# Kernel optimization log

Hardware: AMD Instinct MI355X
Metric: run time of the kernel (lower is better)

## Reference

```python
import jax, jax.numpy as jnp
import numpy as np

B, P, E = 256, 196, 2048           # batch, num_pixels, encoder_size
H, A, EMB = 2048, 512, 300         # hidden, attention, embedding dims
V_IN, V_OUT = 262, 261             # input vocab (classes+2), output (classes+1)
T = 7                              # max_seq_len + 2


def setup_inputs() -> dict:
    key = jax.random.key(0)
    ks = jax.random.split(key, 20)
    s = 0.02
    return {
        "encoder_feature_out": jax.random.normal(ks[0], (B, P, E), jnp.float32),
        "encoder_out": jax.random.normal(ks[1], (B, E), jnp.float32),
        "annotations_X": jax.random.randint(ks[2], (B, T), 0, V_IN),
        "is_train": 1,
        "emb_W": jax.random.normal(ks[3], (V_IN, EMB), jnp.float32) * s,
        "feat_W": jax.random.normal(ks[4], (H, E), jnp.float32) * s,
        "feat_b": jnp.zeros((H,), jnp.float32),
        "W_ih": jax.random.normal(ks[5], (4 * H, EMB + E), jnp.float32) * s,
        "W_hh": jax.random.normal(ks[6], (4 * H, H), jnp.float32) * s,
        "b_ih": jnp.zeros((4 * H,), jnp.float32),
        "b_hh": jnp.zeros((4 * H,), jnp.float32),
        "enc_att_W": jax.random.normal(ks[7], (A, E), jnp.float32) * s,
        "enc_att_b": jnp.zeros((A,), jnp.float32),
        "dec_att_W": jax.random.normal(ks[8], (A, H), jnp.float32) * s,
        "dec_att_b": jnp.zeros((A,), jnp.float32),
        "full_att_W": jax.random.normal(ks[9], (1, A), jnp.float32) * s,
        "full_att_b": jnp.zeros((1,), jnp.float32),
        "fbeta_W": jax.random.normal(ks[10], (E, H), jnp.float32) * s,
        "fbeta_b": jnp.zeros((E,), jnp.float32),
        "fc_W": jax.random.normal(ks[11], (V_OUT, H), jnp.float32) * s,
        "fc_b": jnp.zeros((V_OUT,), jnp.float32),
    }


def _forward(encoder_feature_out, encoder_out, annotations_X,
             emb_W, feat_W, feat_b, W_ih, W_hh, b_ih, b_hh,
             enc_att_W, enc_att_b, dec_att_W, dec_att_b,
             full_att_W, full_att_b, fbeta_W, fbeta_b, fc_W, fc_b):
    enc = encoder_feature_out                                  # (B,P,E)
    # encoder side of additive attention is constant across steps
    att1 = jnp.einsum('bpe,ae->bpa', enc, enc_att_W) + enc_att_b  # (B,P,A)
    h0 = encoder_out @ feat_W.T + feat_b                       # (B,H)
    c0 = jnp.zeros_like(h0)

    def step(carry, ann_t):
        h, c = carry
        # additive attention
        att2 = h @ dec_att_W.T + dec_att_b                     # (B,A)
        e = jax.nn.relu(att1 + att2[:, None, :]) @ full_att_W[0] + full_att_b[0]  # (B,P)
        alpha = jax.nn.softmax(e, axis=1)                      # (B,P)
        awe = jnp.einsum('bp,bpe->be', alpha, enc)             # (B,E)
        gate = jax.nn.sigmoid(h @ fbeta_W.T + fbeta_b)         # (B,E)
        awe = gate * awe
        # LSTMCell (dropout layers in eval mode -> identity)
        x = jnp.concatenate([emb_W[ann_t], awe], axis=1)       # (B,EMB+E)
        gates = x @ W_ih.T + b_ih + h @ W_hh.T + b_hh          # (B,4H)
        i, f, g, o = jnp.split(gates, 4, axis=1)
        c = jax.nn.sigmoid(f) * c + jax.nn.sigmoid(i) * jnp.tanh(g)
        h = jax.nn.sigmoid(o) * jnp.tanh(c)
        yhat = h @ fc_W.T + fc_b                               # (B,V_OUT)
        return (h, c), (yhat, alpha)

    _, (yhats, alphas) = jax.lax.scan(step, (h0, c0), annotations_X.T)  # (T,B,...)
    return jnp.transpose(yhats, (1, 0, 2)), jnp.transpose(alphas, (1, 0, 2))


def reference(encoder_feature_out, encoder_out, annotations_X, is_train,
              emb_W, feat_W, feat_b, W_ih, W_hh, b_ih, b_hh,
              enc_att_W, enc_att_b, dec_att_W, dec_att_b,
              full_att_W, full_att_b, fbeta_W, fbeta_b, fc_W, fc_b):
    # is_train=True (teacher forcing) path
    return _forward(encoder_feature_out, encoder_out, annotations_X,
                    emb_W, feat_W, feat_b, W_ih, W_hh, b_ih, b_hh,
                    enc_att_W, enc_att_b, dec_att_W, dec_att_b,
                    full_att_W, full_att_b, fbeta_W, fbeta_b, fc_W, fc_b)
```

## Files before the change

kernel.cpp:

```cpp
#include <hip/hip_runtime.h>
#include <math.h>

#define B_    256
#define P_    196
#define E_    2048
#define H_    2048
#define A_    512
#define EMB_  300
#define VOUT_ 261
#define T_    7

#define KPAD_   4608
#define EMBOFF_ 2048
#define AWEOFF_ 2352

#define NSTEP_  2880
#define FCOFF_  2560
#define GSPLIT_ 4

typedef __attribute__((ext_vector_type(8))) short          short8_t;
typedef __attribute__((ext_vector_type(8))) unsigned short ushort8_t;
typedef __attribute__((ext_vector_type(4))) float          f32x4;

__device__ __forceinline__ unsigned short f2b(float f) {
    union { float f; unsigned int u; } v; v.f = f;
    unsigned int x = v.u;
    unsigned int r = (x + 0x7fffu + ((x >> 16) & 1u)) >> 16;
    return (unsigned short)r;
}
__device__ __forceinline__ float b2f(unsigned short u) {
    union { unsigned int u; float f; } v; v.u = ((unsigned int)u) << 16;
    return v.f;
}
__device__ __forceinline__ ushort8_t pack8(float4 u0, float4 u1) {
    ushort8_t u;
    u[0]=f2b(u0.x); u[1]=f2b(u0.y); u[2]=f2b(u0.z); u[3]=f2b(u0.w);
    u[4]=f2b(u1.x); u[5]=f2b(u1.y); u[6]=f2b(u1.z); u[7]=f2b(u1.w);
    return u;
}

template<bool SPLITK, bool OUT16, bool XCDSWZ>
__global__ __launch_bounds__(256)
void gemm_sk(const unsigned short* __restrict__ Ab, int lda,
             const unsigned short* __restrict__ Bw, int ldb,
             void* __restrict__ Cout, int ldc,
             int Kper, int colbase, const float* __restrict__ bias, int nbx)
{
    __shared__ ushort8_t As8[256 * 8];
    __shared__ ushort8_t Bs8[64 * 8];

    const int tid  = threadIdx.x;
    const int lane = tid & 63;
    const int w    = tid >> 6;

    int nblk, mblk;
    if (XCDSWZ) {
        const int bid  = blockIdx.x;
        const int pair = (bid & 7) * (gridDim.x >> 3) + (bid >> 3);
        nblk = pair % nbx;
        mblk = pair / nbx;
    } else {
        nblk = blockIdx.x;
        mblk = 0;
    }
    const int col0  = colbase + nblk * 64;
    const int kbase = SPLITK ? blockIdx.y * Kper : 0;
    const int mrow0 = XCDSWZ ? mblk * 256 : 0;

    const int rb  = tid >> 3;
    const int seg = tid & 7;
    const int swz = seg ^ (rb & 7);

    const unsigned short* Ap = Ab + (size_t)(mrow0 + rb) * lda + kbase + seg * 8;
    const unsigned short* Bp = Bw + (size_t)(col0 + rb) * ldb + kbase + seg * 8;

    const int lr = lane & 15;
    const int hi = lane >> 4;

    f32x4 acc[4][4];
    #pragma unroll
    for (int m = 0; m < 4; ++m)
        #pragma unroll
        for (int n = 0; n < 4; ++n)
            acc[m][n] = (f32x4){0.f, 0.f, 0.f, 0.f};

    ushort8_t aR[8], bR[2];
    #pragma unroll
    for (int i = 0; i < 8; ++i)
        aR[i] = *(const ushort8_t*)(Ap + (size_t)i * 32 * lda);
    bR[0] = *(const ushort8_t*)(Bp);
    bR[1] = *(const ushort8_t*)(Bp + (size_t)32 * ldb);

    for (int k0 = 0; k0 < Kper; k0 += 64) {
        __syncthreads();
        #pragma unroll
        for (int i = 0; i < 8; ++i)
            As8[(rb + i * 32) * 8 + swz] = aR[i];
        Bs8[rb * 8 + swz]        = bR[0];
        Bs8[(rb + 32) * 8 + swz] = bR[1];
        __syncthreads();
        if (k0 + 64 < Kper) {
            #pragma unroll
            for (int i = 0; i < 8; ++i)
                aR[i] = *(const ushort8_t*)(Ap + (size_t)i * 32 * lda + k0 + 64);
            bR[0] = *(const ushort8_t*)(Bp + k0 + 64);
            bR[1] = *(const ushort8_t*)(Bp + (size_t)32 * ldb + k0 + 64);
        }
        #pragma unroll
        for (int kc = 0; kc < 2; ++kc) {
            short8_t af[4], bf[4];
            #pragma unroll
            for (int m = 0; m < 4; ++m) {
                const int row = w * 64 + m * 16 + lr;
                af[m] = *(const short8_t*)&As8[row * 8 + ((kc * 4 + hi) ^ (row & 7))];
            }
            #pragma unroll
            for (int n = 0; n < 4; ++n) {
                const int row = n * 16 + lr;
                bf[n] = *(const short8_t*)&Bs8[row * 8 + ((kc * 4 + hi) ^ (row & 7))];
            }
            #pragma unroll
            for (int m = 0; m < 4; ++m)
                #pragma unroll
                for (int n = 0; n < 4; ++n)
                    acc[m][n] = __builtin_amdgcn_mfma_f32_16x16x32_bf16(
                        af[m], bf[n], acc[m][n], 0, 0, 0);
        }
    }

    if (OUT16) {
        unsigned short* C16 = (unsigned short*)Cout;
        #pragma unroll
        for (int m = 0; m < 4; ++m) {
            const int grow0 = mrow0 + w * 64 + m * 16 + hi * 4;
            #pragma unroll
            for (int n = 0; n < 4; ++n) {
                const int gcol = col0 + n * 16 + lr;
                const float bv = bias[gcol];
                #pragma unroll
                for (int r = 0; r < 4; ++r)
                    C16[(size_t)(grow0 + r) * ldc + gcol] = f2b(acc[m][n][r] + bv);
            }
        }
    } else {
        float* Cs = (float*)Cout + (SPLITK ? (size_t)blockIdx.y * 256 * ldc : 0);
        #pragma unroll
        for (int m = 0; m < 4; ++m) {
            const int grow0 = w * 64 + m * 16 + hi * 4;
            #pragma unroll
            for (int n = 0; n < 4; ++n) {
                const int gcol = col0 + n * 16 + lr;
                #pragma unroll
                for (int r = 0; r < 4; ++r)
                    Cs[(size_t)(grow0 + r) * ldc + gcol] = acc[m][n][r];
            }
        }
    }
}

__global__ __launch_bounds__(256)
void gemm_mfma_f32(const float* __restrict__ Af, int lda,
                   const unsigned short* __restrict__ Bw, int ldb,
                   unsigned short* __restrict__ Cp, int ldc,
                   const float* __restrict__ bias,
                   int M, int N, int K)
{
    __shared__ __align__(16) unsigned short As[64][40];
    __shared__ __align__(16) unsigned short Bs[128][40];

    const int tid  = threadIdx.x;
    const int lane = tid & 63;
    const int wid  = tid >> 6;
    const int wr   = wid >> 1;
    const int wc   = wid & 1;
    const int row0 = blockIdx.y * 64;
    const int col0 = blockIdx.x * 128;

    const int ar = tid >> 2;
    const int as = (tid & 3) * 8;
    const int br = tid >> 1;
    const int bs = (tid & 1) * 16;

    const int lr = lane & 15;
    const int lk = (lane >> 4) * 8;

    f32x4 acc[2][4];
    #pragma unroll
    for (int m = 0; m < 2; ++m)
        #pragma unroll
        for (int n = 0; n < 4; ++n)
            acc[m][n] = (f32x4){0.f, 0.f, 0.f, 0.f};

    for (int k0 = 0; k0 < K; k0 += 32) {
        ushort8_t aval = {0,0,0,0,0,0,0,0};
        if (row0 + ar < M) {
            const float* p = Af + (size_t)(row0 + ar) * lda + k0 + as;
            aval = pack8(*(const float4*)(p), *(const float4*)(p + 4));
        }
        ushort8_t bv0 = {0,0,0,0,0,0,0,0}, bv1 = {0,0,0,0,0,0,0,0};
        if (col0 + br < N) {
            const unsigned short* p = Bw + (size_t)(col0 + br) * ldb + k0 + bs;
            bv0 = *(const ushort8_t*)(p);
            bv1 = *(const ushort8_t*)(p + 8);
        }
        __syncthreads();
        *(ushort8_t*)&As[ar][as]     = aval;
        *(ushort8_t*)&Bs[br][bs]     = bv0;
        *(ushort8_t*)&Bs[br][bs + 8] = bv1;
        __syncthreads();

        short8_t af[2], bf[4];
        #pragma unroll
        for (int m = 0; m < 2; ++m)
            af[m] = *(const short8_t*)&As[wr * 32 + m * 16 + lr][lk];
        #pragma unroll
        for (int n = 0; n < 4; ++n)
            bf[n] = *(const short8_t*)&Bs[wc * 64 + n * 16 + lr][lk];
        #pragma unroll
        for (int m = 0; m < 2; ++m)
            #pragma unroll
            for (int n = 0; n < 4; ++n)
                acc[m][n] = __builtin_amdgcn_mfma_f32_16x16x32_bf16(
                    af[m], bf[n], acc[m][n], 0, 0, 0);
    }

    #pragma unroll
    for (int m = 0; m < 2; ++m) {
        const int grow0 = row0 + wr * 32 + m * 16 + (lane >> 4) * 4;
        #pragma unroll
        for (int n = 0; n < 4; ++n) {
            const int gcol = col0 + wc * 64 + n * 16 + lr;
            if (gcol >= N) continue;
            const float bv = bias[gcol];
            #pragma unroll
            for (int r = 0; r < 4; ++r) {
                const int grow = grow0 + r;
                if (grow >= M) continue;
                Cp[(size_t)grow * ldc + gcol] = f2b(acc[m][n][r] + bv);
            }
        }
    }
}

__global__ __launch_bounds__(256)
void cvt_bf16_kernel(const float* __restrict__ in, unsigned short* __restrict__ out,
                     int n8)
{
    const int idx = blockIdx.x * 256 + threadIdx.x;
    if (idx >= n8) return;
    const size_t base = (size_t)idx * 8;
    *(ushort8_t*)(out + base) =
        pack8(*(const float4*)(in + base), *(const float4*)(in + base + 4));
}

__global__ __launch_bounds__(256)
void build_wcat_kernel(const float* __restrict__ W_ih, const float* __restrict__ W_hh,
                       unsigned short* __restrict__ wcat)
{
    const int row = blockIdx.x;
    const int LIH = EMB_ + E_;
    for (int s = threadIdx.x; s < KPAD_ / 8; s += 256) {
        const int k0 = s * 8;
        ushort8_t u;
        const float* src = nullptr;
        if (k0 + 8 <= H_)                         src = W_hh + (size_t)row * H_ + k0;
        else if (k0 >= H_ && k0 + 8 <= 2344)      src = W_ih + (size_t)row * LIH + (k0 - H_);
        else if (k0 >= AWEOFF_ && k0 + 8 <= 4400) src = W_ih + (size_t)row * LIH + (k0 - 2052);
        if (src) {
            u = pack8(*(const float4*)(src), *(const float4*)(src + 4));
        } else {
            #pragma unroll
            for (int i = 0; i < 8; ++i) {
                const int k = k0 + i;
                float v = 0.f;
                if (k >= H_ && k < 2348)           v = W_ih[(size_t)row * LIH + (k - H_)];
                else if (k >= AWEOFF_ && k < 4400) v = W_ih[(size_t)row * LIH + (k - 2052)];
                u[i] = f2b(v);
            }
        }
        *(ushort8_t*)(wcat + (size_t)row * KPAD_ + k0) = u;
    }
}

__global__ __launch_bounds__(256)
void build_wstep_kernel(const float* __restrict__ dec_attW,
                        const float* __restrict__ fbeta_W,
                        const float* __restrict__ fc_W,
                        unsigned short* __restrict__ wstep)
{
    const int row = blockIdx.x;
    const int c0  = threadIdx.x * 8;
    const float* src;
    if (row < A_)                   src = dec_attW + (size_t)row * H_ + c0;
    else if (row < A_ + E_)         src = fbeta_W + (size_t)(row - A_) * H_ + c0;
    else if (row < A_ + E_ + VOUT_) src = fc_W + (size_t)(row - A_ - E_) * H_ + c0;
    else                            src = nullptr;
    ushort8_t u = {0,0,0,0,0,0,0,0};
    if (src) u = pack8(*(const float4*)(src), *(const float4*)(src + 4));
    *(ushort8_t*)(wstep + (size_t)row * H_ + c0) = u;
}

__global__ __launch_bounds__(256)
void reduce_h0(const float* __restrict__ parts, const float* __restrict__ bias,
               unsigned short* __restrict__ xcat)
{
    const int i = blockIdx.x * 256 + threadIdx.x;
    const int row = i >> 11, col = i & (H_ - 1);
    float acc = bias[col];
    #pragma unroll
    for (int s = 0; s < 8; ++s)
        acc += parts[(size_t)s * 256 * H_ + i];
    xcat[(size_t)row * KPAD_ + col] = f2b(acc);
}

__global__ __launch_bounds__(256)
void fused_att(const float* __restrict__ parts, const float* __restrict__ dec_attb,
               const unsigned short* __restrict__ att1,
               const float* __restrict__ fw_g, const float* __restrict__ fb,
               float* __restrict__ alpha, float* __restrict__ out_a, int t)
{
    const int b = blockIdx.x;
    const int tid = threadIdx.x;
    const int lane = tid & 63;
    const int wid  = tid >> 6;
    __shared__ float att2s[A_];
    __shared__ float es[P_];
    __shared__ float red[4];

    #pragma unroll
    for (int it = 0; it < A_ / 256; ++it) {
        const int c = tid + it * 256;
        float acc = dec_attb[c];
        #pragma unroll
        for (int s = 0; s < 8; ++s)
            acc += parts[((size_t)s * B_ + b) * NSTEP_ + c];
        att2s[c] = acc;
    }
    __syncthreads();

    const int l32  = lane & 31;
    const int slot = wid * 2 + (lane >> 5);
    float a2r[16], fwr[16];
    #pragma unroll
    for (int k = 0; k < 16; ++k) {
        a2r[k] = att2s[l32 * 16 + k];
        fwr[k] = fw_g[l32 * 16 + k];
    }
    const float fbv = fb[0];

    for (int p = slot; p < P_; p += 8) {
        const unsigned short* row = att1 + ((size_t)b * P_ + p) * A_ + l32 * 16;
        ushort8_t v0 = *(const ushort8_t*)(row);
        ushort8_t v1 = *(const ushort8_t*)(row + 8);
        float acc = 0.f;
        #pragma unroll
        for (int k = 0; k < 8; ++k) {
            float x = b2f(v0[k]) + a2r[k];
            x = x > 0.f ? x : 0.f;
            acc = fmaf(x, fwr[k], acc);
        }
        #pragma unroll
        for (int k = 0; k < 8; ++k) {
            float x = b2f(v1[k]) + a2r[k + 8];
            x = x > 0.f ? x : 0.f;
            acc = fmaf(x, fwr[k + 8], acc);
        }
        #pragma unroll
        for (int off = 16; off > 0; off >>= 1)
            acc += __shfl_xor(acc, off);
        if (l32 == 0) es[p] = acc + fbv;
    }
    __syncthreads();

    float v = (tid < P_) ? es[tid] : -1e30f;
    float m = v;
    #pragma unroll
    for (int off = 32; off > 0; off >>= 1)
        m = fmaxf(m, __shfl_xor(m, off));
    if (lane == 0) red[wid] = m;
    __syncthreads();
    m = fmaxf(fmaxf(red[0], red[1]), fmaxf(red[2], red[3]));
    __syncthreads();
    float p = (tid < P_) ? expf(v - m) : 0.f;
    float s = p;
    #pragma unroll
    for (int off = 32; off > 0; off >>= 1)
        s += __shfl_xor(s, off);
    if (lane == 0) red[wid] = s;
    __syncthreads();
    s = red[0] + red[1] + red[2] + red[3];
    if (tid < P_) {
        const float a = p / s;
        alpha[b * P_ + tid] = a;
        out_a[((size_t)b * T_ + t) * P_ + tid] = a;
    }
}

__global__ __launch_bounds__(256)
void fused_awe(const float* __restrict__ parts, const float* __restrict__ fbeta_b,
               const float* __restrict__ alpha,
               const float* __restrict__ encf, const unsigned short* __restrict__ enc16,
               int use16,
               const int* __restrict__ ann, const float* __restrict__ embW,
               unsigned short* __restrict__ xcat,
               const float* __restrict__ fc_b, float* __restrict__ out_y, int t)
{
    const int b = blockIdx.x;
    const int tid = threadIdx.x;
    __shared__ float al[P_];
    if (tid < P_) al[tid] = alpha[b * P_ + tid];
    __syncthreads();

    const int e0 = tid * 8;
    float g[8];
    #pragma unroll
    for (int k = 0; k < 8; ++k) {
        float acc = fbeta_b[e0 + k];
        #pragma unroll
        for (int s = 0; s < 8; ++s)
            acc += parts[((size_t)s * B_ + b) * NSTEP_ + A_ + e0 + k];
        g[k] = 1.f / (1.f + expf(-acc));
    }

    float acc[8] = {0.f,0.f,0.f,0.f,0.f,0.f,0.f,0.f};
    if (use16) {
        const unsigned short* ep = enc16 + (size_t)b * P_ * E_ + e0;
        for (int p = 0; p < P_; p += 4) {
            ushort8_t v0 = *(const ushort8_t*)(ep + (size_t)(p + 0) * E_);
            ushort8_t v1 = *(const ushort8_t*)(ep + (size_t)(p + 1) * E_);
            ushort8_t v2 = *(const ushort8_t*)(ep + (size_t)(p + 2) * E_);
            ushort8_t v3 = *(const ushort8_t*)(ep + (size_t)(p + 3) * E_);
            const float a0 = al[p], a1 = al[p + 1], a2 = al[p + 2], a3 = al[p + 3];
            #pragma unroll
            for (int k = 0; k < 8; ++k) {
                float t0 = fmaf(a0, b2f(v0[k]), acc[k]);
                float t1 = fmaf(a1, b2f(v1[k]), t0);
                float t2 = fmaf(a2, b2f(v2[k]), t1);
                acc[k]   = fmaf(a3, b2f(v3[k]), t2);
            }
        }
    } else {
        const float* ep = encf + (size_t)b * P_ * E_ + e0;
        for (int p = 0; p < P_; ++p) {
            float4 v0 = *(const float4*)(ep + (size_t)p * E_);
            float4 v1 = *(const float4*)(ep + (size_t)p * E_ + 4);
            const float a0 = al[p];
            acc[0] = fmaf(a0, v0.x, acc[0]); acc[1] = fmaf(a0, v0.y, acc[1]);
            acc[2] = fmaf(a0, v0.z, acc[2]); acc[3] = fmaf(a0, v0.w, acc[3]);
            acc[4] = fmaf(a0, v1.x, acc[4]); acc[5] = fmaf(a0, v1.y, acc[5]);
            acc[6] = fmaf(a0, v1.z, acc[6]); acc[7] = fmaf(a0, v1.w, acc[7]);
        }
    }
    ushort8_t o;
    #pragma unroll
    for (int k = 0; k < 8; ++k) o[k] = f2b(g[k] * acc[k]);
    *(ushort8_t*)(xcat + (size_t)b * KPAD_ + AWEOFF_ + e0) = o;

    const int r = ann[b * T_ + t];
    for (int j = tid; j < EMB_; j += 256)
        xcat[(size_t)b * KPAD_ + EMBOFF_ + j] = f2b(embW[(size_t)r * EMB_ + j]);

    if (t > 0) {
        for (int c = tid; c < VOUT_; c += 256) {
            float a = fc_b[c];
            #pragma unroll
            for (int s = 0; s < 8; ++s)
                a += parts[((size_t)s * B_ + b) * NSTEP_ + FCOFF_ + c];
            out_y[((size_t)b * T_ + (t - 1)) * VOUT_ + c] = a;
        }
    }
}

__global__ __launch_bounds__(256)
void fc_reduce(const float* __restrict__ parts, const float* __restrict__ fc_b,
               float* __restrict__ out_y, int tm1)
{
    const int i = blockIdx.x * 256 + threadIdx.x;
    if (i >= B_ * VOUT_) return;
    const int b = i / VOUT_;
    const int c = i - b * VOUT_;
    float acc = fc_b[c];
    #pragma unroll
    for (int s = 0; s < 8; ++s)
        acc += parts[((size_t)s * B_ + b) * NSTEP_ + FCOFF_ + c];
    out_y[((size_t)b * T_ + tm1) * VOUT_ + c] = acc;
}

__global__ __launch_bounds__(256)
void lstm_kernel(const float* __restrict__ parts, const float* __restrict__ bias4h,
                 float* __restrict__ c, unsigned short* __restrict__ xcat)
{
    const int idx = blockIdx.x * 256 + threadIdx.x;
    const int b = idx >> 11;
    const int j = idx & (H_ - 1);
    const float* p0 = parts + (size_t)b * 4 * H_;
    const size_t S = (size_t)256 * 4 * H_;
    float gi = bias4h[j],          gf = bias4h[H_ + j];
    float gg = bias4h[2 * H_ + j], go = bias4h[3 * H_ + j];
    #pragma unroll
    for (int s = 0; s < GSPLIT_; ++s) {
        const float* p = p0 + s * S;
        gi += p[j]; gf += p[H_ + j]; gg += p[2 * H_ + j]; go += p[3 * H_ + j];
    }
    const float si = 1.f / (1.f + expf(-gi));
    const float sf = 1.f / (1.f + expf(-gf));
    const float so = 1.f / (1.f + expf(-go));
    const float cn = sf * c[idx] + si * tanhf(gg);
    c[idx] = cn;
    xcat[(size_t)b * KPAD_ + j] = f2b(so * tanhf(cn));
}

__global__ __launch_bounds__(256)
void addvec_kernel(const float* __restrict__ a, const float* __restrict__ b,
                   float* __restrict__ o, int n)
{
    const int i = blockIdx.x * 256 + threadIdx.x;
    if (i < n) o[i] = a[i] + b[i];
}

extern "C" void kernel_launch(void* const* d_in, const int* in_sizes, int n_in,
                              void* d_out, int out_size, void* d_ws, size_t ws_size,
                              hipStream_t stream)
{
    const float* enc      = (const float*)d_in[0];
    const float* enc_out  = (const float*)d_in[1];
    const int*   ann      = (const int*)  d_in[2];
    const float* emb_W    = (const float*)d_in[4];
    const float* feat_W   = (const float*)d_in[5];
    const float* feat_b   = (const float*)d_in[6];
    const float* W_ih     = (const float*)d_in[7];
    const float* W_hh     = (const float*)d_in[8];
    const float* b_ih     = (const float*)d_in[9];
    const float* b_hh     = (const float*)d_in[10];
    const float* enc_attW = (const float*)d_in[11];
    const float* enc_attb = (const float*)d_in[12];
    const float* dec_attW = (const float*)d_in[13];
    const float* dec_attb = (const float*)d_in[14];
    const float* full_attW= (const float*)d_in[15];
    const float* full_attb= (const float*)d_in[16];
    const float* fbeta_W  = (const float*)d_in[17];
    const float* fbeta_b  = (const float*)d_in[18];
    const float* fc_W     = (const float*)d_in[19];
    const float* fc_b     = (const float*)d_in[20];
    (void)in_sizes; (void)n_in; (void)out_size;

    float* out   = (float*)d_out;
    float* out_y = out;
    float* out_a = out + (size_t)B_ * T_ * VOUT_;

    char* base = (char*)d_ws;
    size_t off = 0;
    auto alloc = [&](size_t bytes) -> char* {
        char* p = base + off;
        off += (bytes + 255) & ~(size_t)255;
        return p;
    };
    unsigned short* att1_16   = (unsigned short*)alloc((size_t)B_ * P_ * A_ * 2);
    unsigned short* wcat16    = (unsigned short*)alloc((size_t)4 * H_ * KPAD_ * 2);
    unsigned short* wstep16   = (unsigned short*)alloc((size_t)NSTEP_ * H_ * 2);
    unsigned short* encattW16 = (unsigned short*)alloc((size_t)A_ * E_ * 2);
    unsigned short* featW16   = (unsigned short*)alloc((size_t)H_ * E_ * 2);
    unsigned short* encout16  = (unsigned short*)alloc((size_t)B_ * E_ * 2);
    unsigned short* xcat16    = (unsigned short*)alloc((size_t)B_ * KPAD_ * 2);
    float* cbuf    = (float*)alloc((size_t)B_ * H_ * 4);
    float* alpha   = (float*)alloc((size_t)B_ * P_ * 4);
    float* bias4h  = (float*)alloc((size_t)4 * H_ * 4);
    const size_t parts_elems = (size_t)GSPLIT_ * B_ * 4 * H_;
    float* parts   = (float*)alloc(parts_elems * 4);
    const size_t enc_elems = (size_t)B_ * P_ * E_;
    const int use16 = (off + enc_elems * 2 <= ws_size) ? 1 : 0;
    unsigned short* enc16 = use16 ? (unsigned short*)alloc(enc_elems * 2) : nullptr;

    const dim3 blk(256);

    addvec_kernel<<<dim3((4 * H_ + 255) / 256), blk, 0, stream>>>(b_ih, b_hh, bias4h, 4 * H_);
    cvt_bf16_kernel<<<dim3((A_ * E_ / 8 + 255) / 256), blk, 0, stream>>>(enc_attW, encattW16, A_ * E_ / 8);
    cvt_bf16_kernel<<<dim3((H_ * E_ / 8 + 255) / 256), blk, 0, stream>>>(feat_W, featW16, H_ * E_ / 8);
    cvt_bf16_kernel<<<dim3((B_ * E_ / 8 + 255) / 256), blk, 0, stream>>>(enc_out, encout16, B_ * E_ / 8);
    build_wcat_kernel<<<dim3(4 * H_), blk, 0, stream>>>(W_ih, W_hh, wcat16);
    build_wstep_kernel<<<dim3(NSTEP_), blk, 0, stream>>>(dec_attW, fbeta_W, fc_W, wstep16);
    hipMemsetAsync(xcat16, 0, (size_t)B_ * KPAD_ * 2, stream);
    hipMemsetAsync(cbuf, 0, (size_t)B_ * H_ * 4, stream);
    if (use16)
        cvt_bf16_kernel<<<dim3((int)(enc_elems / 8 + 255) / 256), blk, 0, stream>>>(
            enc, enc16, (int)(enc_elems / 8));

    if (use16) {
        gemm_sk<false, true, true><<<dim3(196 * 8), blk, 0, stream>>>(
            enc16, E_, encattW16, E_, att1_16, A_, E_, 0, enc_attb, 8);
    } else {
        dim3 g((A_ + 127) / 128, (B_ * P_) / 64);
        gemm_mfma_f32<<<g, blk, 0, stream>>>(enc, E_, encattW16, E_,
            att1_16, A_, enc_attb, B_ * P_, A_, E_);
    }
    gemm_sk<true, false, false><<<dim3(H_ / 64, 8), blk, 0, stream>>>(
        encout16, E_, featW16, E_, parts, H_, E_ / 8, 0, nullptr, 0);
    reduce_h0<<<dim3(B_ * H_ / 256), blk, 0, stream>>>(parts, feat_b, xcat16);

    for (int t = 0; t <= T_; ++t) {
        if (t < T_)
            gemm_sk<true, false, false><<<dim3(NSTEP_ / 64, 8), blk, 0, stream>>>(
                xcat16, KPAD_, wstep16, H_, parts, NSTEP_, H_ / 8, 0, nullptr, 0);
        else
            gemm_sk<true, false, false><<<dim3((NSTEP_ - FCOFF_) / 64, 8), blk, 0, stream>>>(
                xcat16, KPAD_, wstep16, H_, parts, NSTEP_, H_ / 8, FCOFF_, nullptr, 0);
        if (t == T_) {
            fc_reduce<<<dim3((B_ * VOUT_ + 255) / 256), blk, 0, stream>>>(parts, fc_b, out_y, t - 1);
            break;
        }

        fused_att<<<dim3(B_), blk, 0, stream>>>(parts, dec_attb, att1_16,
                                                full_attW, full_attb, alpha, out_a, t);
        fused_awe<<<dim3(B_), blk, 0, stream>>>(parts, fbeta_b, alpha, enc, enc16,
                                                use16, ann, emb_W, xcat16,
                                                fc_b, out_y, t);

        gemm_sk<true, false, false><<<dim3(4 * H_ / 64, GSPLIT_), blk, 0, stream>>>(
            xcat16, KPAD_, wcat16, KPAD_, parts, 4 * H_, KPAD_ / GSPLIT_, 0, nullptr, 0);
        lstm_kernel<<<dim3(B_ * H_ / 256), blk, 0, stream>>>(parts, bias4h, cbuf, xcat16);
    }
}
```

Baseline: 1.226 ms.

## Split attention-weighted encoding across pixel halves and widen att1 GEMM tile

The fused attention-weighted-encoding kernel is split in two. One kernel computes partial sums over two halves of the pixel range, using 2×B blocks instead of B, and a second kernel reduces the halves and applies the sigmoid gate. This is meant to give more parallelism to the bandwidth-bound encoder read in each step. Separately, the gemm kernel gains a template parameter for N tile width, and the one-time encoder attention projection now uses 128-wide tiles to improve A-tile reuse. Costs are an extra launch per step, an extra buffer round-trip, and more registers in the wider GEMM.

```diff
diff --git a/kernel.cpp b/kernel.cpp
--- a/kernel.cpp
+++ b/kernel.cpp
@@ -39,15 +39,17 @@
     return u;
 }
 
-template<bool SPLITK, bool OUT16, bool XCDSWZ>
+template<bool SPLITK, bool OUT16, bool XCDSWZ, int BN>
 __global__ __launch_bounds__(256)
 void gemm_sk(const unsigned short* __restrict__ Ab, int lda,
              const unsigned short* __restrict__ Bw, int ldb,
              void* __restrict__ Cout, int ldc,
              int Kper, int colbase, const float* __restrict__ bias, int nbx)
 {
+    constexpr int NB32 = BN / 32;
+    constexpr int NF   = BN / 16;
     __shared__ ushort8_t As8[256 * 8];
-    __shared__ ushort8_t Bs8[64 * 8];
+    __shared__ ushort8_t Bs8[BN * 8];
 
     const int tid  = threadIdx.x;
     const int lane = tid & 63;
@@ -63,7 +65,7 @@
         nblk = blockIdx.x;
         mblk = 0;
     }
-    const int col0  = colbase + nblk * 64;
+    const int col0  = colbase + nblk * BN;
     const int kbase = SPLITK ? blockIdx.y * Kper : 0;
     const int mrow0 = XCDSWZ ? mblk * 256 : 0;
 
@@ -77,52 +79,55 @@
     const int lr = lane & 15;
     const int hi = lane >> 4;
 
-    f32x4 acc[4][4];
+    f32x4 acc[4][NF];
     #pragma unroll
     for (int m = 0; m < 4; ++m)
         #pragma unroll
-        for (int n = 0; n < 4; ++n)
+        for (int n = 0; n < NF; ++n)
             acc[m][n] = (f32x4){0.f, 0.f, 0.f, 0.f};
 
-    ushort8_t aR[8], bR[2];
+    ushort8_t aR[8], bR[NB32];
     #pragma unroll
     for (int i = 0; i < 8; ++i)
         aR[i] = *(const ushort8_t*)(Ap + (size_t)i * 32 * lda);
-    bR[0] = *(const ushort8_t*)(Bp);
-    bR[1] = *(const ushort8_t*)(Bp + (size_t)32 * ldb);
+    #pragma unroll
+    for (int j = 0; j < NB32; ++j)
+        bR[j] = *(const ushort8_t*)(Bp + (size_t)j * 32 * ldb);
 
     for (int k0 = 0; k0 < Kper; k0 += 64) {
         __syncthreads();
         #pragma unroll
         for (int i = 0; i < 8; ++i)
             As8[(rb + i * 32) * 8 + swz] = aR[i];
-        Bs8[rb * 8 + swz]        = bR[0];
-        Bs8[(rb + 32) * 8 + swz] = bR[1];
+        #pragma unroll
+        for (int j = 0; j < NB32; ++j)
+            Bs8[(rb + j * 32) * 8 + swz] = bR[j];
         __syncthreads();
         if (k0 + 64 < Kper) {
             #pragma unroll
             for (int i = 0; i < 8; ++i)
                 aR[i] = *(const ushort8_t*)(Ap + (size_t)i * 32 * lda + k0 + 64);
-            bR[0] = *(const ushort8_t*)(Bp + k0 + 64);
-            bR[1] = *(const ushort8_t*)(Bp + (size_t)32 * ldb + k0 + 64);
+            #pragma unroll
+            for (int j = 0; j < NB32; ++j)
+                bR[j] = *(const ushort8_t*)(Bp + (size_t)j * 32 * ldb + k0 + 64);
         }
         #pragma unroll
         for (int kc = 0; kc < 2; ++kc) {
-            short8_t af[4], bf[4];
+            short8_t af[4], bf[NF];
             #pragma unroll
             for (int m = 0; m < 4; ++m) {
                 const int row = w * 64 + m * 16 + lr;
                 af[m] = *(const short8_t*)&As8[row * 8 + ((kc * 4 + hi) ^ (row & 7))];
             }
             #pragma unroll
-            for (int n = 0; n < 4; ++n) {
+            for (int n = 0; n < NF; ++n) {
                 const int row = n * 16 + lr;
                 bf[n] = *(const short8_t*)&Bs8[row * 8 + ((kc * 4 + hi) ^ (row & 7))];
             }
             #pragma unroll
             for (int m = 0; m < 4; ++m)
                 #pragma unroll
-                for (int n = 0; n < 4; ++n)
+                for (int n = 0; n < NF; ++n)
                     acc[m][n] = __builtin_amdgcn_mfma_f32_16x16x32_bf16(
                         af[m], bf[n], acc[m][n], 0, 0, 0);
         }
@@ -134,7 +139,7 @@
         for (int m = 0; m < 4; ++m) {
             const int grow0 = mrow0 + w * 64 + m * 16 + hi * 4;
             #pragma unroll
-            for (int n = 0; n < 4; ++n) {
+            for (int n = 0; n < NF; ++n) {
                 const int gcol = col0 + n * 16 + lr;
                 const float bv = bias[gcol];
                 #pragma unroll
@@ -148,7 +153,7 @@
         for (int m = 0; m < 4; ++m) {
             const int grow0 = w * 64 + m * 16 + hi * 4;
             #pragma unroll
-            for (int n = 0; n < 4; ++n) {
+            for (int n = 0; n < NF; ++n) {
                 const int gcol = col0 + n * 16 + lr;
                 #pragma unroll
                 for (int r = 0; r < 4; ++r)
@@ -397,35 +402,24 @@
 }
 
 __global__ __launch_bounds__(256)
-void fused_awe(const float* __restrict__ parts, const float* __restrict__ fbeta_b,
-               const float* __restrict__ alpha,
-               const float* __restrict__ encf, const unsigned short* __restrict__ enc16,
-               int use16,
-               const int* __restrict__ ann, const float* __restrict__ embW,
-               unsigned short* __restrict__ xcat,
-               const float* __restrict__ fc_b, float* __restrict__ out_y, int t)
-{
-    const int b = blockIdx.x;
+void awe_part_kernel(const float* __restrict__ alpha,
+                     const float* __restrict__ encf,
+                     const unsigned short* __restrict__ enc16, int use16,
+                     float* __restrict__ awe_part)
+{
+    const int ph = blockIdx.x;
+    const int b  = blockIdx.y;
     const int tid = threadIdx.x;
-    __shared__ float al[P_];
-    if (tid < P_) al[tid] = alpha[b * P_ + tid];
+    __shared__ float al[98];
+    if (tid < 98) al[tid] = alpha[b * P_ + ph * 98 + tid];
     __syncthreads();
 
     const int e0 = tid * 8;
-    float g[8];
-    #pragma unroll
-    for (int k = 0; k < 8; ++k) {
-        float acc = fbeta_b[e0 + k];
-        #pragma unroll
-        for (int s = 0; s < 8; ++s)
-            acc += parts[((size_t)s * B_ + b) * NSTEP_ + A_ + e0 + k];
-        g[k] = 1.f / (1.f + expf(-acc));
-    }
-
     float acc[8] = {0.f,0.f,0.f,0.f,0.f,0.f,0.f,0.f};
     if (use16) {
-        const unsigned short* ep = enc16 + (size_t)b * P_ * E_ + e0;
-        for (int p = 0; p < P_; p += 4) {
+        const unsigned short* ep = enc16 + ((size_t)b * P_ + ph * 98) * E_ + e0;
+        int p = 0;
+        for (; p + 4 <= 98; p += 4) {
             ushort8_t v0 = *(const ushort8_t*)(ep + (size_t)(p + 0) * E_);
             ushort8_t v1 = *(const ushort8_t*)(ep + (size_t)(p + 1) * E_);
             ushort8_t v2 = *(const ushort8_t*)(ep + (size_t)(p + 2) * E_);
@@ -439,9 +433,16 @@
                 acc[k]   = fmaf(a3, b2f(v3[k]), t2);
             }
         }
+        for (; p < 98; ++p) {
+            ushort8_t v0 = *(const ushort8_t*)(ep + (size_t)p * E_);
+            const float a0 = al[p];
+            #pragma unroll
+            for (int k = 0; k < 8; ++k)
+                acc[k] = fmaf(a0, b2f(v0[k]), acc[k]);
+        }
     } else {
-        const float* ep = encf + (size_t)b * P_ * E_ + e0;
-        for (int p = 0; p < P_; ++p) {
+        const float* ep = encf + ((size_t)b * P_ + ph * 98) * E_ + e0;
+        for (int p = 0; p < 98; ++p) {
             float4 v0 = *(const float4*)(ep + (size_t)p * E_);
             float4 v1 = *(const float4*)(ep + (size_t)p * E_ + 4);
             const float a0 = al[p];
@@ -451,9 +452,39 @@
             acc[6] = fmaf(a0, v1.z, acc[6]); acc[7] = fmaf(a0, v1.w, acc[7]);
         }
     }
+    float* dst = awe_part + ((size_t)ph * B_ + b) * E_ + e0;
+    *(float4*)(dst)     = make_float4(acc[0], acc[1], acc[2], acc[3]);
+    *(float4*)(dst + 4) = make_float4(acc[4], acc[5], acc[6], acc[7]);
+}
+
+__global__ __launch_bounds__(256)
+void awe_fin_kernel(const float* __restrict__ parts, const float* __restrict__ fbeta_b,
+                    const float* __restrict__ awe_part,
+                    const int* __restrict__ ann, const float* __restrict__ embW,
+                    unsigned short* __restrict__ xcat,
+                    const float* __restrict__ fc_b, float* __restrict__ out_y, int t)
+{
+    const int b = blockIdx.x;
+    const int tid = threadIdx.x;
+    const int e0 = tid * 8;
+
+    float4 p0a = *(const float4*)(awe_part + (size_t)b * E_ + e0);
+    float4 p0b = *(const float4*)(awe_part + (size_t)b * E_ + e0 + 4);
+    float4 p1a = *(const float4*)(awe_part + ((size_t)B_ + b) * E_ + e0);
+    float4 p1b = *(const float4*)(awe_part + ((size_t)B_ + b) * E_ + e0 + 4);
+    float aw[8] = {p0a.x + p1a.x, p0a.y + p1a.y, p0a.z + p1a.z, p0a.w + p1a.w,
+                   p0b.x + p1b.x, p0b.y + p1b.y, p0b.z + p1b.z, p0b.w + p1b.w};
+
     ushort8_t o;
     #pragma unroll
-    for (int k = 0; k < 8; ++k) o[k] = f2b(g[k] * acc[k]);
+    for (int k = 0; k < 8; ++k) {
+        float g = fbeta_b[e0 + k];
+        #pragma unroll
+        for (int s = 0; s < 8; ++s)
+            g += parts[((size_t)s * B_ + b) * NSTEP_ + A_ + e0 + k];
+        const float sg = 1.f / (1.f + expf(-g));
+        o[k] = f2b(sg * aw[k]);
+    }
     *(ushort8_t*)(xcat + (size_t)b * KPAD_ + AWEOFF_ + e0) = o;
 
     const int r = ann[b * T_ + t];
@@ -562,9 +593,10 @@
     unsigned short* featW16   = (unsigned short*)alloc((size_t)H_ * E_ * 2);
     unsigned short* encout16  = (unsigned short*)alloc((size_t)B_ * E_ * 2);
     unsigned short* xcat16    = (unsigned short*)alloc((size_t)B_ * KPAD_ * 2);
-    float* cbuf    = (float*)alloc((size_t)B_ * H_ * 4);
-    float* alpha   = (float*)alloc((size_t)B_ * P_ * 4);
-    float* bias4h  = (float*)alloc((size_t)4 * H_ * 4);
+    float* cbuf     = (float*)alloc((size_t)B_ * H_ * 4);
+    float* alpha    = (float*)alloc((size_t)B_ * P_ * 4);
+    float* bias4h   = (float*)alloc((size_t)4 * H_ * 4);
+    float* awe_part = (float*)alloc((size_t)2 * B_ * E_ * 4);
     const size_t parts_elems = (size_t)GSPLIT_ * B_ * 4 * H_;
     float* parts   = (float*)alloc(parts_elems * 4);
     const size_t enc_elems = (size_t)B_ * P_ * E_;
@@ -586,23 +618,23 @@
             enc, enc16, (int)(enc_elems / 8));
 
     if (use16) {
-        gemm_sk<false, true, true><<<dim3(196 * 8), blk, 0, stream>>>(
-            enc16, E_, encattW16, E_, att1_16, A_, E_, 0, enc_attb, 8);
+        gemm_sk<false, true, true, 128><<<dim3(196 * 4), blk, 0, stream>>>(
+            enc16, E_, encattW16, E_, att1_16, A_, E_, 0, enc_attb, 4);
     } else {
         dim3 g((A_ + 127) / 128, (B_ * P_) / 64);
         gemm_mfma_f32<<<g, blk, 0, stream>>>(enc, E_, encattW16, E_,
             att1_16, A_, enc_attb, B_ * P_, A_, E_);
     }
-    gemm_sk<true, false, false><<<dim3(H_ / 64, 8), blk, 0, stream>>>(
+    gemm_sk<true, false, false, 64><<<dim3(H_ / 64, 8), blk, 0, stream>>>(
         encout16, E_, featW16, E_, parts, H_, E_ / 8, 0, nullptr, 0);
     reduce_h0<<<dim3(B_ * H_ / 256), blk, 0, stream>>>(parts, feat_b, xcat16);
 
     for (int t = 0; t <= T_; ++t) {
         if (t < T_)
-            gemm_sk<true, false, false><<<dim3(NSTEP_ / 64, 8), blk, 0, stream>>>(
+            gemm_sk<true, false, false, 64><<<dim3(NSTEP_ / 64, 8), blk, 0, stream>>>(
                 xcat16, KPAD_, wstep16, H_, parts, NSTEP_, H_ / 8, 0, nullptr, 0);
         else
-            gemm_sk<true, false, false><<<dim3((NSTEP_ - FCOFF_) / 64, 8), blk, 0, stream>>>(
+            gemm_sk<true, false, false, 64><<<dim3((NSTEP_ - FCOFF_) / 64, 8), blk, 0, stream>>>(
                 xcat16, KPAD_, wstep16, H_, parts, NSTEP_, H_ / 8, FCOFF_, nullptr, 0);
         if (t == T_) {
             fc_reduce<<<dim3((B_ * VOUT_ + 255) / 256), blk, 0, stream>>>(parts, fc_b, out_y, t - 1);
@@ -611,11 +643,11 @@
 
         fused_att<<<dim3(B_), blk, 0, stream>>>(parts, dec_attb, att1_16,
                                                 full_attW, full_attb, alpha, out_a, t);
-        fused_awe<<<dim3(B_), blk, 0, stream>>>(parts, fbeta_b, alpha, enc, enc16,
-                                                use16, ann, emb_W, xcat16,
-                                                fc_b, out_y, t);
-
-        gemm_sk<true, false, false><<<dim3(4 * H_ / 64, GSPLIT_), blk, 0, stream>>>(
+        awe_part_kernel<<<dim3(2, B_), blk, 0, stream>>>(alpha, enc, enc16, use16, awe_part);
+        awe_fin_kernel<<<dim3(B_), blk, 0, stream>>>(parts, fbeta_b, awe_part,
+                                                     ann, emb_W, xcat16, fc_b, out_y, t);
+
+        gemm_sk<true, false, false, 64><<<dim3(4 * H_ / 64, GSPLIT_), blk, 0, stream>>>(
             xcat16, KPAD_, wcat16, KPAD_, parts, 4 * H_, KPAD_ / GSPLIT_, 0, nullptr, 0);
         lstm_kernel<<<dim3(B_ * H_ / 256), blk, 0, stream>>>(parts, bias4h, cbuf, xcat16);
     }
```

Measured after the change: 1.254 ms. 2.3% more time.

## Fuse attention softmax with weighted-sum over split pixel halves; merge setup kernels

Applied to the files above, without the earlier changes.

The attention-score/softmax kernel now also computes the attention-weighted encoder sum, with the grid split into two pixel halves per batch row so 512 blocks run instead of 256. A small finishing kernel adds the two partial sums, applies the sigmoid gate and writes the LSTM input, which removes the alpha round trip through global memory. Each half-block recomputes the full softmax, so that work is duplicated. Separately, the bias add, weight conversions and buffer memsets are merged into one setup kernel to cut launch count.

```diff
diff --git a/kernel.cpp b/kernel.cpp
--- a/kernel.cpp
+++ b/kernel.cpp
@@ -17,6 +17,7 @@
 #define NSTEP_  2880
 #define FCOFF_  2560
 #define GSPLIT_ 4
+#define PSPLIT_ 2
 
 typedef __attribute__((ext_vector_type(8))) short          short8_t;
 typedef __attribute__((ext_vector_type(8))) unsigned short ushort8_t;
@@ -251,6 +252,72 @@
     const size_t base = (size_t)idx * 8;
     *(ushort8_t*)(out + base) =
         pack8(*(const float4*)(in + base), *(const float4*)(in + base + 4));
+}
+
+__global__ __launch_bounds__(256)
+void setup_kernel(const float* __restrict__ b_ih, const float* __restrict__ b_hh,
+                  float* __restrict__ bias4h,
+                  const float* __restrict__ enc_attW, unsigned short* __restrict__ encattW16,
+                  const float* __restrict__ feat_W, unsigned short* __restrict__ featW16,
+                  const float* __restrict__ enc_out, unsigned short* __restrict__ encout16,
+                  const float* __restrict__ dec_attW, const float* __restrict__ fbeta_W,
+                  const float* __restrict__ fc_W, unsigned short* __restrict__ wstep,
+                  unsigned short* __restrict__ xcat, float* __restrict__ cbuf)
+{
+    int bid = blockIdx.x;
+    const int tid = threadIdx.x;
+    if (bid < 32) {
+        const int i = bid * 256 + tid;
+        bias4h[i] = b_ih[i] + b_hh[i];
+        return;
+    }
+    bid -= 32;
+    if (bid < 512) {
+        const size_t base = ((size_t)bid * 256 + tid) * 8;
+        *(ushort8_t*)(encattW16 + base) =
+            pack8(*(const float4*)(enc_attW + base), *(const float4*)(enc_attW + base + 4));
+        return;
+    }
+    bid -= 512;
+    if (bid < 2048) {
+        const size_t base = ((size_t)bid * 256 + tid) * 8;
+        *(ushort8_t*)(featW16 + base) =
+            pack8(*(const float4*)(feat_W + base), *(const float4*)(feat_W + base + 4));
+        return;
+    }
+    bid -= 2048;
+    if (bid < 256) {
+        const size_t base = ((size_t)bid * 256 + tid) * 8;
+        *(ushort8_t*)(encout16 + base) =
+            pack8(*(const float4*)(enc_out + base), *(const float4*)(enc_out + base + 4));
+        return;
+    }
+    bid -= 256;
+    if (bid < NSTEP_) {
+        const int row = bid;
+        const int c0  = tid * 8;
+        const float* src;
+        if (row < A_)                   src = dec_attW + (size_t)row * H_ + c0;
+        else if (row < A_ + E_)         src = fbeta_W + (size_t)(row - A_) * H_ + c0;
+        else if (row < A_ + E_ + VOUT_) src = fc_W + (size_t)(row - A_ - E_) * H_ + c0;
+        else                            src = nullptr;
+        ushort8_t u = {0,0,0,0,0,0,0,0};
+        if (src) u = pack8(*(const float4*)(src), *(const float4*)(src + 4));
+        *(ushort8_t*)(wstep + (size_t)row * H_ + c0) = u;
+        return;
+    }
+    bid -= NSTEP_;
+    if (bid < 576) {
+        const size_t base = ((size_t)bid * 256 + tid) * 8;
+        ushort8_t z = {0,0,0,0,0,0,0,0};
+        *(ushort8_t*)(xcat + base) = z;
+        return;
+    }
+    bid -= 576;
+    {
+        const size_t base = ((size_t)bid * 256 + tid) * 4;
+        *(float4*)(cbuf + base) = make_float4(0.f, 0.f, 0.f, 0.f);
+    }
 }
 
 __global__ __launch_bounds__(256)
@@ -283,24 +350,6 @@
 }
 
 __global__ __launch_bounds__(256)
-void build_wstep_kernel(const float* __restrict__ dec_attW,
-                        const float* __restrict__ fbeta_W,
-                        const float* __restrict__ fc_W,
-                        unsigned short* __restrict__ wstep)
-{
-    const int row = blockIdx.x;
-    const int c0  = threadIdx.x * 8;
-    const float* src;
-    if (row < A_)                   src = dec_attW + (size_t)row * H_ + c0;
-    else if (row < A_ + E_)         src = fbeta_W + (size_t)(row - A_) * H_ + c0;
-    else if (row < A_ + E_ + VOUT_) src = fc_W + (size_t)(row - A_ - E_) * H_ + c0;
-    else                            src = nullptr;
-    ushort8_t u = {0,0,0,0,0,0,0,0};
-    if (src) u = pack8(*(const float4*)(src), *(const float4*)(src + 4));
-    *(ushort8_t*)(wstep + (size_t)row * H_ + c0) = u;
-}
-
-__global__ __launch_bounds__(256)
 void reduce_h0(const float* __restrict__ parts, const float* __restrict__ bias,
                unsigned short* __restrict__ xcat)
 {
@@ -314,12 +363,15 @@
 }
 
 __global__ __launch_bounds__(256)
-void fused_att(const float* __restrict__ parts, const float* __restrict__ dec_attb,
-               const unsigned short* __restrict__ att1,
-               const float* __restrict__ fw_g, const float* __restrict__ fb,
-               float* __restrict__ alpha, float* __restrict__ out_a, int t)
-{
-    const int b = blockIdx.x;
+void att_awe_kernel(const float* __restrict__ parts, const float* __restrict__ dec_attb,
+                    const unsigned short* __restrict__ att1,
+                    const float* __restrict__ fw_g, const float* __restrict__ fb,
+                    const float* __restrict__ encf, const unsigned short* __restrict__ enc16,
+                    int use16,
+                    float* __restrict__ awe_part, float* __restrict__ out_a, int t)
+{
+    const int ph = blockIdx.x;
+    const int b  = blockIdx.y;
     const int tid = threadIdx.x;
     const int lane = tid & 63;
     const int wid  = tid >> 6;
@@ -389,48 +441,28 @@
     if (lane == 0) red[wid] = s;
     __syncthreads();
     s = red[0] + red[1] + red[2] + red[3];
+    float alv = p / s;
     if (tid < P_) {
-        const float a = p / s;
-        alpha[b * P_ + tid] = a;
-        out_a[((size_t)b * T_ + t) * P_ + tid] = a;
-    }
-}
-
-__global__ __launch_bounds__(256)
-void fused_awe(const float* __restrict__ parts, const float* __restrict__ fbeta_b,
-               const float* __restrict__ alpha,
-               const float* __restrict__ encf, const unsigned short* __restrict__ enc16,
-               int use16,
-               const int* __restrict__ ann, const float* __restrict__ embW,
-               unsigned short* __restrict__ xcat,
-               const float* __restrict__ fc_b, float* __restrict__ out_y, int t)
-{
-    const int b = blockIdx.x;
-    const int tid = threadIdx.x;
-    __shared__ float al[P_];
-    if (tid < P_) al[tid] = alpha[b * P_ + tid];
+        if (ph == 0)
+            out_a[((size_t)b * T_ + t) * P_ + tid] = alv;
+    }
     __syncthreads();
+    if (tid < P_) es[tid] = alv;
+    __syncthreads();
 
     const int e0 = tid * 8;
-    float g[8];
-    #pragma unroll
-    for (int k = 0; k < 8; ++k) {
-        float acc = fbeta_b[e0 + k];
-        #pragma unroll
-        for (int s = 0; s < 8; ++s)
-            acc += parts[((size_t)s * B_ + b) * NSTEP_ + A_ + e0 + k];
-        g[k] = 1.f / (1.f + expf(-acc));
-    }
-
+    const int prow0 = ph * 98;
     float acc[8] = {0.f,0.f,0.f,0.f,0.f,0.f,0.f,0.f};
     if (use16) {
-        const unsigned short* ep = enc16 + (size_t)b * P_ * E_ + e0;
-        for (int p = 0; p < P_; p += 4) {
-            ushort8_t v0 = *(const ushort8_t*)(ep + (size_t)(p + 0) * E_);
-            ushort8_t v1 = *(const ushort8_t*)(ep + (size_t)(p + 1) * E_);
-            ushort8_t v2 = *(const ushort8_t*)(ep + (size_t)(p + 2) * E_);
-            ushort8_t v3 = *(const ushort8_t*)(ep + (size_t)(p + 3) * E_);
-            const float a0 = al[p], a1 = al[p + 1], a2 = al[p + 2], a3 = al[p + 3];
+        const unsigned short* ep = enc16 + ((size_t)b * P_ + prow0) * E_ + e0;
+        int pp = 0;
+        for (; pp + 4 <= 98; pp += 4) {
+            ushort8_t v0 = *(const ushort8_t*)(ep + (size_t)(pp + 0) * E_);
+            ushort8_t v1 = *(const ushort8_t*)(ep + (size_t)(pp + 1) * E_);
+            ushort8_t v2 = *(const ushort8_t*)(ep + (size_t)(pp + 2) * E_);
+            ushort8_t v3 = *(const ushort8_t*)(ep + (size_t)(pp + 3) * E_);
+            const float a0 = es[prow0 + pp],     a1 = es[prow0 + pp + 1];
+            const float a2 = es[prow0 + pp + 2], a3 = es[prow0 + pp + 3];
             #pragma unroll
             for (int k = 0; k < 8; ++k) {
                 float t0 = fmaf(a0, b2f(v0[k]), acc[k]);
@@ -439,21 +471,60 @@
                 acc[k]   = fmaf(a3, b2f(v3[k]), t2);
             }
         }
+        for (; pp < 98; ++pp) {
+            ushort8_t v0 = *(const ushort8_t*)(ep + (size_t)pp * E_);
+            const float a0 = es[prow0 + pp];
+            #pragma unroll
+            for (int k = 0; k < 8; ++k)
+                acc[k] = fmaf(a0, b2f(v0[k]), acc[k]);
+        }
     } else {
-        const float* ep = encf + (size_t)b * P_ * E_ + e0;
-        for (int p = 0; p < P_; ++p) {
-            float4 v0 = *(const float4*)(ep + (size_t)p * E_);
-            float4 v1 = *(const float4*)(ep + (size_t)p * E_ + 4);
-            const float a0 = al[p];
+        const float* ep = encf + ((size_t)b * P_ + prow0) * E_ + e0;
+        for (int pp = 0; pp < 98; ++pp) {
+            float4 v0 = *(const float4*)(ep + (size_t)pp * E_);
+            float4 v1 = *(const float4*)(ep + (size_t)pp * E_ + 4);
+            const float a0 = es[prow0 + pp];
             acc[0] = fmaf(a0, v0.x, acc[0]); acc[1] = fmaf(a0, v0.y, acc[1]);
             acc[2] = fmaf(a0, v0.z, acc[2]); acc[3] = fmaf(a0, v0.w, acc[3]);
             acc[4] = fmaf(a0, v1.x, acc[4]); acc[5] = fmaf(a0, v1.y, acc[5]);
             acc[6] = fmaf(a0, v1.z, acc[6]); acc[7] = fmaf(a0, v1.w, acc[7]);
         }
     }
+    float* dst = awe_part + ((size_t)ph * B_ + b) * E_ + e0;
+    *(float4*)(dst)     = make_float4(acc[0], acc[1], acc[2], acc[3]);
+    *(float4*)(dst + 4) = make_float4(acc[4], acc[5], acc[6], acc[7]);
+}
+
+__global__ __launch_bounds__(256)
+void awe_fin_kernel(const float* __restrict__ parts, const float* __restrict__ fbeta_b,
+                    const float* __restrict__ awe_part,
+                    const int* __restrict__ ann, const float* __restrict__ embW,
+                    unsigned short* __restrict__ xcat,
+                    const float* __restrict__ fc_b, float* __restrict__ out_y, int t)
+{
+    const int b = blockIdx.x;
+    const int tid = threadIdx.x;
+    const int e0 = tid * 8;
+
+    float aw[8] = {0.f,0.f,0.f,0.f,0.f,0.f,0.f,0.f};
+    #pragma unroll
+    for (int ph = 0; ph < PSPLIT_; ++ph) {
+        float4 pa = *(const float4*)(awe_part + ((size_t)ph * B_ + b) * E_ + e0);
+        float4 pb = *(const float4*)(awe_part + ((size_t)ph * B_ + b) * E_ + e0 + 4);
+        aw[0] += pa.x; aw[1] += pa.y; aw[2] += pa.z; aw[3] += pa.w;
+        aw[4] += pb.x; aw[5] += pb.y; aw[6] += pb.z; aw[7] += pb.w;
+    }
+
     ushort8_t o;
     #pragma unroll
-    for (int k = 0; k < 8; ++k) o[k] = f2b(g[k] * acc[k]);
+    for (int k = 0; k < 8; ++k) {
+        float g = fbeta_b[e0 + k];
+        #pragma unroll
+        for (int s = 0; s < 8; ++s)
+            g += parts[((size_t)s * B_ + b) * NSTEP_ + A_ + e0 + k];
+        const float sg = 1.f / (1.f + expf(-g));
+        o[k] = f2b(sg * aw[k]);
+    }
     *(ushort8_t*)(xcat + (size_t)b * KPAD_ + AWEOFF_ + e0) = o;
 
     const int r = ann[b * T_ + t];
@@ -508,14 +579,6 @@
     const float cn = sf * c[idx] + si * tanhf(gg);
     c[idx] = cn;
     xcat[(size_t)b * KPAD_ + j] = f2b(so * tanhf(cn));
-}
-
-__global__ __launch_bounds__(256)
-void addvec_kernel(const float* __restrict__ a, const float* __restrict__ b,
-                   float* __restrict__ o, int n)
-{
-    const int i = blockIdx.x * 256 + threadIdx.x;
-    if (i < n) o[i] = a[i] + b[i];
 }
 
 extern "C" void kernel_launch(void* const* d_in, const int* in_sizes, int n_in,
@@ -562,9 +625,9 @@
     unsigned short* featW16   = (unsigned short*)alloc((size_t)H_ * E_ * 2);
     unsigned short* encout16  = (unsigned short*)alloc((size_t)B_ * E_ * 2);
     unsigned short* xcat16    = (unsigned short*)alloc((size_t)B_ * KPAD_ * 2);
-    float* cbuf    = (float*)alloc((size_t)B_ * H_ * 4);
-    float* alpha   = (float*)alloc((size_t)B_ * P_ * 4);
-    float* bias4h  = (float*)alloc((size_t)4 * H_ * 4);
+    float* cbuf     = (float*)alloc((size_t)B_ * H_ * 4);
+    float* bias4h   = (float*)alloc((size_t)4 * H_ * 4);
+    float* awe_part = (float*)alloc((size_t)PSPLIT_ * B_ * E_ * 4);
     const size_t parts_elems = (size_t)GSPLIT_ * B_ * 4 * H_;
     float* parts   = (float*)alloc(parts_elems * 4);
     const size_t enc_elems = (size_t)B_ * P_ * E_;
@@ -573,14 +636,10 @@
 
     const dim3 blk(256);
 
-    addvec_kernel<<<dim3((4 * H_ + 255) / 256), blk, 0, stream>>>(b_ih, b_hh, bias4h, 4 * H_);
-    cvt_bf16_kernel<<<dim3((A_ * E_ / 8 + 255) / 256), blk, 0, stream>>>(enc_attW, encattW16, A_ * E_ / 8);
-    cvt_bf16_kernel<<<dim3((H_ * E_ / 8 + 255) / 256), blk, 0, stream>>>(feat_W, featW16, H_ * E_ / 8);
-    cvt_bf16_kernel<<<dim3((B_ * E_ / 8 + 255) / 256), blk, 0, stream>>>(enc_out, encout16, B_ * E_ / 8);
+    setup_kernel<<<dim3(32 + 512 + 2048 + 256 + NSTEP_ + 576 + 512), blk, 0, stream>>>(
+        b_ih, b_hh, bias4h, enc_attW, encattW16, feat_W, featW16,
+        enc_out, encout16, dec_attW, fbeta_W, fc_W, wstep16, xcat16, cbuf);
     build_wcat_kernel<<<dim3(4 * H_), blk, 0, stream>>>(W_ih, W_hh, wcat16);
-    build_wstep_kernel<<<dim3(NSTEP_), blk, 0, stream>>>(dec_attW, fbeta_W, fc_W, wstep16);
-    hipMemsetAsync(xcat16, 0, (size_t)B_ * KPAD_ * 2, stream);
-    hipMemsetAsync(cbuf, 0, (size_t)B_ * H_ * 4, stream);
     if (use16)
         cvt_bf16_kernel<<<dim3((int)(enc_elems / 8 + 255) / 256), blk, 0, stream>>>(
             enc, enc16, (int)(enc_elems / 8));
@@ -609,11 +668,11 @@
             break;
         }
 
-        fused_att<<<dim3(B_), blk, 0, stream>>>(parts, dec_attb, att1_16,
-                                                full_attW, full_attb, alpha, out_a, t);
-        fused_awe<<<dim3(B_), blk, 0, stream>>>(parts, fbeta_b, alpha, enc, enc16,
-                                                use16, ann, emb_W, xcat16,
-                                                fc_b, out_y, t);
+        att_awe_kernel<<<dim3(PSPLIT_, B_), blk, 0, stream>>>(
+            parts, dec_attb, att1_16, full_attW, full_attb,
+            enc, enc16, use16, awe_part, out_a, t);
+        awe_fin_kernel<<<dim3(B_), blk, 0, stream>>>(parts, fbeta_b, awe_part,
+                                                     ann, emb_W, xcat16, fc_b, out_y, t);
 
         gemm_sk<true, false, false><<<dim3(4 * H_ / 64, GSPLIT_), blk, 0, stream>>>(
             xcat16, KPAD_, wcat16, KPAD_, parts, 4 * H_, KPAD_ / GSPLIT_, 0, nullptr, 0);
```

Result: faster. 1.197 ms (-2.3%).
